# Performance work log

Measured on AMD Instinct MI355X. Metric: run time of the kernel, lower is better.

Reference implementation:

```python
import jax, jax.numpy as jnp
import numpy as np

# Fuzzy system constants (from _init_fuzzy_system)
X1_C = jnp.arange(5.0)                 # x1 gauss centers 0,1,2,3,4 ; sigma 1
X2_C = jnp.arange(5.0) * 45.0          # x2 gauss centers 0,45,90,135,180 ; sigma 45
OUT_C = jnp.array([-0.3, 0.1, 0.5, 0.9, 1.3], dtype=jnp.float32)  # consequent centers ; sigma 0.3
Z = jnp.asarray(np.arange(-0.3, 1.31, 0.01), dtype=jnp.float32)   # 161-pt output universe

# Mamdani rules: list per consequent level of (x1_level, x2_level) OR-terms, levels XS..XL = 0..4
RULES = [
    [(2, 4), (3, 4), (3, 3), (4, 3), (4, 4)],            # -> coupling XS
    [(1, 4), (2, 3), (3, 2), (4, 1)],                    # -> S
    [(0, 4), (1, 3), (2, 2), (3, 1), (4, 0)],            # -> M
    [(0, 3), (1, 2), (2, 1), (3, 0)],                    # -> L
    [(0, 2), (0, 1), (0, 0), (1, 1), (1, 0), (2, 0)],    # -> XL
]


def gauss(x, c, s):
    return jnp.exp(-0.5 * ((x - c) / s) ** 2)


def setup_inputs() -> dict:
    key = jax.random.key(0)
    k1, k2, k3, k4 = jax.random.split(key, 4)
    N, E, D = 50000, 1000000, 8
    h = jax.random.normal(k1, (N, D), dtype=jnp.float32)
    src_idx = jax.random.randint(k2, (E,), 0, N, dtype=jnp.int32)
    dst_idx = jax.random.randint(k3, (E,), 0, N, dtype=jnp.int32)
    etypes = jax.random.randint(k4, (E,), 0, 3, dtype=jnp.int32)
    return {"h": h, "src_idx": src_idx, "dst_idx": dst_idx, "etypes": etypes}


def reference(h, src_idx, dst_idx, etypes):
    # edge vector: dst['h'] - src['h']
    v = h[dst_idx] - h[src_idx]                       # [E, D]
    # Ante_generator: x1 = |v| (distance, clipped to universe), x2 = angle(v, e1) in degrees
    n = jnp.sqrt(jnp.sum(v * v, axis=-1) + 1e-12)     # [E]
    x1 = jnp.clip(n, 0.0, 4.0)
    cosang = jnp.clip(v[:, 0] / n, -0.999999, 0.999999)
    x2 = jnp.degrees(jnp.arccos(cosang))              # [E] in [0, 180]
    # antecedent memberships
    mu1 = gauss(x1[:, None], X1_C[None, :], 1.0)      # [E, 5]
    mu2 = gauss(x2[:, None], X2_C[None, :], 45.0)     # [E, 5]
    zmf = gauss(Z[None, :], OUT_C[:, None], 0.3)      # [5, 161]
    # Mamdani: rule activation = max over OR-terms of min(mu1, mu2);
    # implication = min(act, consequent mf); aggregation = max over rules
    agg = jnp.zeros((x1.shape[0], Z.shape[0]), dtype=h.dtype)  # [E, 161]
    for r, pairs in enumerate(RULES):
        act = jnp.max(
            jnp.stack([jnp.minimum(mu1[:, i], mu2[:, j]) for i, j in pairs], axis=-1),
            axis=-1,
        )                                             # [E]
        agg = jnp.maximum(agg, jnp.minimum(act[:, None], zmf[r][None, :]))
    # centroid defuzzification
    coupling_degree = jnp.sum(agg * Z[None, :], axis=-1) / jnp.sum(agg, axis=-1)
    return coupling_degree
```

## Files before the change

kernel.cpp:

```cpp
#include <hip/hip_runtime.h>
#include <hip/hip_fp16.h>

static constexpr double cexp_taylor(double x) {
    double s = 1.0, t = 1.0;
    for (int i = 1; i < 40; ++i) { t = t * x / (double)i; s += t; }
    return s;
}
static constexpr double cpow_int(double b, long e) {
    double r = 1.0, p = b;
    while (e > 0) { if (e & 1) r *= p; p *= p; e >>= 1; }
    return r;
}
struct ZmfTab { float v[5][161]; };
static constexpr ZmfTab make_zmf() {
    ZmfTab t{};
    const double c0 = cexp_taylor(-1.0 / 1800.0);
    for (int r = 0; r < 5; ++r)
        for (int k = 0; k < 161; ++k) {
            long d = (long)(k - 40 * r);
            t.v[r][k] = (float)cpow_int(c0, d * d);
        }
    return t;
}
static constexpr ZmfTab ZMF = make_zmf();
static constexpr float ZCUT = 1e-4f;

__device__ __forceinline__ float fuzzy_F(float x1, float u)
{
    float m1[5], m2[5];
#pragma unroll
    for (int i = 0; i < 5; ++i) {
        float d1 = x1 - (float)i;
        float d2 = u  - (float)i;
        m1[i] = __expf(-0.5f * d1 * d1);
        m2[i] = __expf(-0.5f * d2 * d2);
    }

    float a0 = fmaxf(fmaxf(fminf(m1[2], m2[4]), fminf(m1[3], m2[4])),
               fmaxf(fminf(m1[3], m2[3]),
               fmaxf(fminf(m1[4], m2[3]), fminf(m1[4], m2[4]))));
    float a1 = fmaxf(fmaxf(fminf(m1[1], m2[4]), fminf(m1[2], m2[3])),
               fmaxf(fminf(m1[3], m2[2]), fminf(m1[4], m2[1])));
    float a2 = fmaxf(fmaxf(fminf(m1[0], m2[4]), fminf(m1[1], m2[3])),
               fmaxf(fminf(m1[2], m2[2]),
               fmaxf(fminf(m1[3], m2[1]), fminf(m1[4], m2[0]))));
    float a3 = fmaxf(fmaxf(fminf(m1[0], m2[3]), fminf(m1[1], m2[2])),
               fmaxf(fminf(m1[2], m2[1]), fminf(m1[3], m2[0])));
    float a4 = fmaxf(fmaxf(fmaxf(fminf(m1[0], m2[2]), fminf(m1[0], m2[1])),
               fmaxf(fminf(m1[0], m2[0]), fminf(m1[1], m2[1]))),
               fmaxf(fminf(m1[1], m2[0]), fminf(m1[2], m2[0])));
    float a[5] = {a0, a1, a2, a3, a4};

    float s0 = 0.0f, s1 = 0.0f;
#pragma unroll
    for (int k = 0; k < 161; ++k) {
        float m = -1.0f;
        bool first = true;
#pragma unroll
        for (int r = 0; r < 5; ++r) {
            if (ZMF.v[r][k] >= ZCUT) {
                float tmin = fminf(a[r], ZMF.v[r][k]);
                m = first ? tmin : fmaxf(m, tmin);
                first = false;
            }
        }
        s0 += m;
        s1 = fmaf(m, (float)k, s1);
    }
    return fmaf(0.01f, s1 / s0, -0.3f);
}

#define GN 256

__global__ __launch_bounds__(256) void build_table_kernel(float* __restrict__ tabf)
{
    int idx = blockIdx.x * blockDim.x + threadIdx.x;
    int i1 = idx >> 8;
    int i2 = idx & 255;
    const float hstep = 4.0f / 255.0f;
    float f = fuzzy_F((float)i1 * hstep, (float)i2 * hstep);

    tabf[4 * idx + 0] = f;
    if (i2 > 0)           tabf[4 * (idx - 1)   + 1] = f;
    if (i1 > 0)           tabf[4 * (idx - GN)  + 2] = f;
    if (i1 > 0 && i2 > 0) tabf[4 * (idx - GN - 1) + 3] = f;
}

__global__ __launch_bounds__(256) void pack_h_kernel(
    const float4* __restrict__ h4, __half2* __restrict__ hp, int N)
{
    int r = blockIdx.x * blockDim.x + threadIdx.x;
    if (r >= N) return;
    float4 a = h4[2 * r], b = h4[2 * r + 1];
    __half2* o = hp + 4 * r;
    o[0] = __floats2half2_rn(a.x, a.y);
    o[1] = __floats2half2_rn(a.z, a.w);
    o[2] = __floats2half2_rn(b.x, b.y);
    o[3] = __floats2half2_rn(b.z, b.w);
}

struct H8 { __half2 p0, p1, p2, p3; };

__device__ __forceinline__ float edge_eval(
    const H8* __restrict__ hp, const float4* __restrict__ tab4,
    int si, int di)
{
    H8 s = hp[si];
    H8 d = hp[di];

    float2 d0 = __half22float2(__hsub2(d.p0, s.p0));
    float2 d1 = __half22float2(__hsub2(d.p1, s.p1));
    float2 d2 = __half22float2(__hsub2(d.p2, s.p2));
    float2 d3 = __half22float2(__hsub2(d.p3, s.p3));

    float ss = fmaf(d0.x, d0.x, fmaf(d0.y, d0.y, fmaf(d1.x, d1.x, fmaf(d1.y, d1.y,
               fmaf(d2.x, d2.x, fmaf(d2.y, d2.y, fmaf(d3.x, d3.x,
               fmaf(d3.y, d3.y, 1e-12f))))))));

    float rn = rsqrtf(ss);
    float n  = ss * rn;
    float x1 = fminf(n, 4.0f);

    float c = d0.x * rn;
    c = fminf(fmaxf(c, -0.999999f), 0.999999f);

    float ac = fabsf(c);
    float t  = sqrtf(1.0f - ac);
    float p  = fmaf(fmaf(fmaf(-0.0187293f, ac, 0.0742610f), ac, -0.2121144f),
                    ac, 1.5707288f);
    float r0 = t * p;
    float acosv = (c < 0.0f) ? (3.14159265358979f - r0) : r0;
    float u = acosv * 1.27323954473516f;

    const float sc = 255.0f * 0.25f;
    float t1 = x1 * sc;
    float t2 = u  * sc;
    int i1 = min((int)t1, 254);
    int i2 = min((int)t2, 254);
    float f1 = t1 - (float)i1;
    float f2 = t2 - (float)i2;

    float4 patch = tab4[(i1 << 8) + i2];
    float lo = fmaf(f2, patch.y - patch.x, patch.x);
    float hi = fmaf(f2, patch.w - patch.z, patch.z);
    return fmaf(f1, hi - lo, lo);
}

__global__ __launch_bounds__(256) void fuzzy_coupling_kernel(
    const H8*    __restrict__ hp,
    const int*   __restrict__ src,
    const int*   __restrict__ dst,
    const float4* __restrict__ tab4,
    float*       __restrict__ out,
    int E)
{
    int t = blockIdx.x * blockDim.x + threadIdx.x;
    int e0 = 2 * t;
    if (e0 >= E) return;

    if (e0 + 1 < E) {
        int2 sp = ((const int2*)src)[t];
        int2 dp = ((const int2*)dst)[t];
        float r0 = edge_eval(hp, tab4, sp.x, dp.x);
        float r1 = edge_eval(hp, tab4, sp.y, dp.y);
        ((float2*)out)[t] = make_float2(r0, r1);
    } else {
        out[e0] = edge_eval(hp, tab4, src[e0], dst[e0]);
    }
}

extern "C" void kernel_launch(void* const* d_in, const int* in_sizes, int n_in,
                              void* d_out, int out_size, void* d_ws, size_t ws_size,
                              hipStream_t stream)
{
    const float* h   = (const float*)d_in[0];
    const int*   src = (const int*)d_in[1];
    const int*   dst = (const int*)d_in[2];
    float* out = (float*)d_out;

    float*   tabf = (float*)d_ws;
    float4*  tab4 = (float4*)d_ws;
    __half2* hp   = (__half2*)((char*)d_ws + (size_t)GN * GN * 16);

    int N = in_sizes[0] / 8;
    int E = in_sizes[1];

    build_table_kernel<<<(GN * GN) / 256, 256, 0, stream>>>(tabf);
    pack_h_kernel<<<(N + 255) / 256, 256, 0, stream>>>((const float4*)h, hp, N);

    int threads = (E + 1) / 2;
    int grid = (threads + 255) / 256;
    fuzzy_coupling_kernel<<<grid, 256, 0, stream>>>(
        (const H8*)hp, src, dst, tab4, out, E);
}
```

Measured before the change: 84.87 us.

## Shrink lookup table to fp16 80x80 in LDS and fuse setup kernels

```diff
diff --git a/kernel.cpp b/kernel.cpp
--- a/kernel.cpp
+++ b/kernel.cpp
@@ -70,39 +70,42 @@
     return fmaf(0.01f, s1 / s0, -0.3f);
 }
 
-#define GN 256
-
-__global__ __launch_bounds__(256) void build_table_kernel(float* __restrict__ tabf)
-{
-    int idx = blockIdx.x * blockDim.x + threadIdx.x;
-    int i1 = idx >> 8;
-    int i2 = idx & 255;
-    const float hstep = 4.0f / 255.0f;
-    float f = fuzzy_F((float)i1 * hstep, (float)i2 * hstep);
-
-    tabf[4 * idx + 0] = f;
-    if (i2 > 0)           tabf[4 * (idx - 1)   + 1] = f;
-    if (i1 > 0)           tabf[4 * (idx - GN)  + 2] = f;
-    if (i1 > 0 && i2 > 0) tabf[4 * (idx - GN - 1) + 3] = f;
-}
-
-__global__ __launch_bounds__(256) void pack_h_kernel(
-    const float4* __restrict__ h4, __half2* __restrict__ hp, int N)
-{
-    int r = blockIdx.x * blockDim.x + threadIdx.x;
-    if (r >= N) return;
-    float4 a = h4[2 * r], b = h4[2 * r + 1];
-    __half2* o = hp + 4 * r;
-    o[0] = __floats2half2_rn(a.x, a.y);
-    o[1] = __floats2half2_rn(a.z, a.w);
-    o[2] = __floats2half2_rn(b.x, b.y);
-    o[3] = __floats2half2_rn(b.z, b.w);
-}
+#define PN 80
+#define VN 81
+#define TAB_U4 ((PN * PN) / 2)
 
 struct H8 { __half2 p0, p1, p2, p3; };
 
+__global__ __launch_bounds__(256) void build_pack_kernel(
+    const float4* __restrict__ h4, __half* __restrict__ gtab,
+    __half2* __restrict__ hp, int N, int nA)
+{
+    int b = blockIdx.x;
+    if (b < nA) {
+        int idx = b * 256 + threadIdx.x;
+        if (idx >= VN * VN) return;
+        int i = idx / VN;
+        int j = idx - i * VN;
+        const float hstep = 4.0f / (float)PN;
+        __half f = __float2half_rn(fuzzy_F((float)i * hstep, (float)j * hstep));
+        if (i < PN && j < PN) gtab[4 * (i * PN + j) + 0]           = f;
+        if (i < PN && j > 0)  gtab[4 * (i * PN + j - 1) + 1]       = f;
+        if (i > 0 && j < PN)  gtab[4 * ((i - 1) * PN + j) + 2]     = f;
+        if (i > 0 && j > 0)   gtab[4 * ((i - 1) * PN + j - 1) + 3] = f;
+    } else {
+        int r = (b - nA) * 256 + threadIdx.x;
+        if (r >= N) return;
+        float4 a = h4[2 * r], c = h4[2 * r + 1];
+        __half2* o = hp + 4 * r;
+        o[0] = __floats2half2_rn(a.x, a.y);
+        o[1] = __floats2half2_rn(a.z, a.w);
+        o[2] = __floats2half2_rn(c.x, c.y);
+        o[3] = __floats2half2_rn(c.z, c.w);
+    }
+}
+
 __device__ __forceinline__ float edge_eval(
-    const H8* __restrict__ hp, const float4* __restrict__ tab4,
+    const H8* __restrict__ hp, const uint2* __restrict__ stab,
     int si, int di)
 {
     H8 s = hp[si];
@@ -132,40 +135,50 @@
     float acosv = (c < 0.0f) ? (3.14159265358979f - r0) : r0;
     float u = acosv * 1.27323954473516f;
 
-    const float sc = 255.0f * 0.25f;
+    const float sc = (float)PN * 0.25f;
     float t1 = x1 * sc;
     float t2 = u  * sc;
-    int i1 = min((int)t1, 254);
-    int i2 = min((int)t2, 254);
+    int i1 = min((int)t1, PN - 1);
+    int i2 = min((int)t2, PN - 1);
     float f1 = t1 - (float)i1;
     float f2 = t2 - (float)i2;
 
-    float4 patch = tab4[(i1 << 8) + i2];
-    float lo = fmaf(f2, patch.y - patch.x, patch.x);
-    float hi = fmaf(f2, patch.w - patch.z, patch.z);
+    uint2 pk = stab[i1 * PN + i2];
+    float2 lo2 = __half22float2(__builtin_bit_cast(__half2, pk.x));
+    float2 hi2 = __half22float2(__builtin_bit_cast(__half2, pk.y));
+    float lo = fmaf(f2, lo2.y - lo2.x, lo2.x);
+    float hi = fmaf(f2, hi2.y - hi2.x, hi2.x);
     return fmaf(f1, hi - lo, lo);
 }
 
-__global__ __launch_bounds__(256) void fuzzy_coupling_kernel(
+__global__ __launch_bounds__(512) void fuzzy_coupling_kernel(
     const H8*    __restrict__ hp,
     const int*   __restrict__ src,
     const int*   __restrict__ dst,
-    const float4* __restrict__ tab4,
+    const uint4* __restrict__ gtab4,
     float*       __restrict__ out,
     int E)
 {
-    int t = blockIdx.x * blockDim.x + threadIdx.x;
-    int e0 = 2 * t;
+    __shared__ uint4 stab4[TAB_U4];
+    for (int k = threadIdx.x; k < TAB_U4; k += 512) stab4[k] = gtab4[k];
+    __syncthreads();
+    const uint2* stab = (const uint2*)stab4;
+
+    int t = blockIdx.x * 512 + threadIdx.x;
+    int e0 = 4 * t;
     if (e0 >= E) return;
 
-    if (e0 + 1 < E) {
-        int2 sp = ((const int2*)src)[t];
-        int2 dp = ((const int2*)dst)[t];
-        float r0 = edge_eval(hp, tab4, sp.x, dp.x);
-        float r1 = edge_eval(hp, tab4, sp.y, dp.y);
-        ((float2*)out)[t] = make_float2(r0, r1);
+    if (e0 + 3 < E) {
+        int4 sp = ((const int4*)src)[t];
+        int4 dp = ((const int4*)dst)[t];
+        float r0 = edge_eval(hp, stab, sp.x, dp.x);
+        float r1 = edge_eval(hp, stab, sp.y, dp.y);
+        float r2 = edge_eval(hp, stab, sp.z, dp.z);
+        float r3 = edge_eval(hp, stab, sp.w, dp.w);
+        ((float4*)out)[t] = make_float4(r0, r1, r2, r3);
     } else {
-        out[e0] = edge_eval(hp, tab4, src[e0], dst[e0]);
+        for (int e = e0; e < E; ++e)
+            out[e] = edge_eval(hp, stab, src[e], dst[e]);
     }
 }
 
@@ -178,18 +191,19 @@
     const int*   dst = (const int*)d_in[2];
     float* out = (float*)d_out;
 
-    float*   tabf = (float*)d_ws;
-    float4*  tab4 = (float4*)d_ws;
-    __half2* hp   = (__half2*)((char*)d_ws + (size_t)GN * GN * 16);
+    __half*  gtab = (__half*)d_ws;
+    __half2* hp   = (__half2*)((char*)d_ws + 65536);
 
     int N = in_sizes[0] / 8;
     int E = in_sizes[1];
 
-    build_table_kernel<<<(GN * GN) / 256, 256, 0, stream>>>(tabf);
-    pack_h_kernel<<<(N + 255) / 256, 256, 0, stream>>>((const float4*)h, hp, N);
-
-    int threads = (E + 1) / 2;
-    int grid = (threads + 255) / 256;
-    fuzzy_coupling_kernel<<<grid, 256, 0, stream>>>(
-        (const H8*)hp, src, dst, tab4, out, E);
-}
+    int nA = (VN * VN + 255) / 256;
+    int nB = (N + 255) / 256;
+    build_pack_kernel<<<nA + nB, 256, 0, stream>>>(
+        (const float4*)h, gtab, hp, N, nA);
+
+    int threads = (E + 3) / 4;
+    int grid = (threads + 511) / 512;
+    fuzzy_coupling_kernel<<<grid, 512, 0, stream>>>(
+        (const H8*)hp, src, dst, (const uint4*)gtab, out, E);
+}
```

After: 80.60 us. -5.0%, faster.
